# Kernel optimization log

Measured on AMD Instinct MI355X. Metric: run time of the kernel, lower is better.

The kernel has to match this reference:

```python
import jax, jax.numpy as jnp
import numpy as np

IN_CH = 1024
OUT_CH = 1024
N_SUBJECTS = 32
B = 512


def setup_inputs() -> dict:
    key = jax.random.key(0)
    k_x, k_w, k_b, k_idx = jax.random.split(key, 4)
    scale = 1.0 / (IN_CH ** 0.5)
    x = jax.random.normal(k_x, (B, IN_CH), dtype=jnp.float32)
    weights = jax.random.normal(k_w, (N_SUBJECTS, IN_CH, OUT_CH), dtype=jnp.float32) * scale
    bias = jax.random.normal(k_b, (N_SUBJECTS, OUT_CH), dtype=jnp.float32) * scale
    subject_idx = jax.random.randint(k_idx, (B,), 0, N_SUBJECTS, dtype=jnp.int64)
    return {"x": x, "subject_idx": subject_idx, "weights": weights, "bias": bias}


def reference(x, subject_idx, weights, bias):
    # gather per-sample weight [B,C,D] and bias [B,D]
    w = weights[subject_idx]          # [B, C, D]
    b = bias[subject_idx]             # [B, D]
    out = jnp.einsum('bc,bcd->bd', x, w) + b
    return out
```

## Files before the change

### kernel.cpp

```cpp
#include <hip/hip_runtime.h>
#include <hip/hip_bf16.h>


#define N_SUBJ 32
#define B_ROWS 512
#define IN_CH_K 1024
#define OUT_CH_K 1024
#define ROWS_PER_CHUNK 16
#define MAX_CHUNKS 64
#define CSEGS 4
#define CSEG 256
#define DTILES 4
#define DTILE 256

#define ENT_OFF 1
#define PERM_OFF 256
#define PART_OFF_F 1024
#define PART_FLOATS (CSEGS * B_ROWS * OUT_CH_K)
#define WS_NEED_BYTES (4096 + (size_t)PART_FLOATS * 4)

__global__ __launch_bounds__(512) void build_groups(
    const int* __restrict__ idx, int* __restrict__ ws)
{
    __shared__ int counts[N_SUBJ];
    __shared__ int offs[N_SUBJ];
    __shared__ int cursor[N_SUBJ];
    const int t = threadIdx.x;
    if (t < N_SUBJ) counts[t] = 0;
    __syncthreads();
    const int s = idx[t] & (N_SUBJ - 1);
    atomicAdd(&counts[s], 1);
    __syncthreads();
    if (t == 0) {
        int acc = 0, nch = 0;
        for (int i = 0; i < N_SUBJ; ++i) {
            offs[i] = acc;
            cursor[i] = acc;
            acc += counts[i];
        }
        for (int i = 0; i < N_SUBJ; ++i) {
            for (int st = 0; st < counts[i]; st += ROWS_PER_CHUNK) {
                int c = counts[i] - st;
                if (c > ROWS_PER_CHUNK) c = ROWS_PER_CHUNK;
                ws[ENT_OFF + nch * 3 + 0] = i;
                ws[ENT_OFF + nch * 3 + 1] = offs[i] + st;
                ws[ENT_OFF + nch * 3 + 2] = c;
                ++nch;
            }
        }
        ws[0] = nch;
    }
    __syncthreads();
    const int pos = atomicAdd(&cursor[s], 1);
    ws[PERM_OFF + pos] = t;
}

__global__ __launch_bounds__(256) void init_bias(
    const int* __restrict__ idx, const float* __restrict__ bias,
    float* __restrict__ out)
{
    const int b = blockIdx.x;
    const int s = idx[b];
    const int d = threadIdx.x * 4;
    *(float4*)&out[(size_t)b * OUT_CH_K + d] =
        *(const float4*)&bias[(size_t)s * OUT_CH_K + d];
}

template<bool ATOMIC>
__global__ __launch_bounds__(256) void subject_gemm(
    const float* __restrict__ x, const float* __restrict__ W,
    const int* __restrict__ ws, float* __restrict__ ws_part,
    float* __restrict__ out)
{
    const int chunk = blockIdx.x;
    if (chunk >= ws[0]) return;
    const int s     = ws[ENT_OFF + chunk * 3 + 0];
    const int start = ws[ENT_OFF + chunk * 3 + 1];
    const int cnt   = ws[ENT_OFF + chunk * 3 + 2];
    const int cbase = blockIdx.y * CSEG;
    const int dbase = blockIdx.z * DTILE;

    __shared__ float xs[ROWS_PER_CHUNK][CSEG];
    __shared__ int rowidx[ROWS_PER_CHUNK];

    const int t = threadIdx.x;
    if (t < ROWS_PER_CHUNK)
        rowidx[t] = (t < cnt) ? ws[PERM_OFF + start + t] : -1;
    __syncthreads();

    #pragma unroll
    for (int i = 0; i < ROWS_PER_CHUNK; ++i) {
        const int r = rowidx[i];
        xs[i][t] = (r >= 0) ? x[(size_t)r * IN_CH_K + cbase + t] : 0.0f;
    }
    __syncthreads();

    const int lane = t & 63;
    const int wave = t >> 6;
    const int d    = dbase + lane * 4;
    const int r0   = wave * 4;

    float4 acc0 = make_float4(0.f, 0.f, 0.f, 0.f);
    float4 acc1 = make_float4(0.f, 0.f, 0.f, 0.f);
    float4 acc2 = make_float4(0.f, 0.f, 0.f, 0.f);
    float4 acc3 = make_float4(0.f, 0.f, 0.f, 0.f);

    const float* wbase = W + ((size_t)s * IN_CH_K * OUT_CH_K)
                           + (size_t)cbase * OUT_CH_K + d;

    for (int cb = 0; cb < CSEG; cb += 8) {
        float4 wbuf[8];
        #pragma unroll
        for (int j = 0; j < 8; ++j)
            wbuf[j] = *(const float4*)(wbase + (size_t)(cb + j) * OUT_CH_K);
        #pragma unroll
        for (int j = 0; j < 8; ++j) {
            const float xv0 = xs[r0 + 0][cb + j];
            const float xv1 = xs[r0 + 1][cb + j];
            const float xv2 = xs[r0 + 2][cb + j];
            const float xv3 = xs[r0 + 3][cb + j];
            const float4 w4 = wbuf[j];
            acc0.x += xv0 * w4.x; acc0.y += xv0 * w4.y;
            acc0.z += xv0 * w4.z; acc0.w += xv0 * w4.w;
            acc1.x += xv1 * w4.x; acc1.y += xv1 * w4.y;
            acc1.z += xv1 * w4.z; acc1.w += xv1 * w4.w;
            acc2.x += xv2 * w4.x; acc2.y += xv2 * w4.y;
            acc2.z += xv2 * w4.z; acc2.w += xv2 * w4.w;
            acc3.x += xv3 * w4.x; acc3.y += xv3 * w4.y;
            acc3.z += xv3 * w4.z; acc3.w += xv3 * w4.w;
        }
    }

    float4 accs[4] = {acc0, acc1, acc2, acc3};
    #pragma unroll
    for (int r = 0; r < 4; ++r) {
        const int rr = r0 + r;
        if (rr < cnt) {
            const size_t row = (size_t)rowidx[rr];
            if (ATOMIC) {
                float* o = &out[row * OUT_CH_K + d];
                atomicAdd(o + 0, accs[r].x);
                atomicAdd(o + 1, accs[r].y);
                atomicAdd(o + 2, accs[r].z);
                atomicAdd(o + 3, accs[r].w);
            } else {
                *(float4*)&ws_part[((size_t)blockIdx.y * B_ROWS + row)
                                   * OUT_CH_K + d] = accs[r];
            }
        }
    }
}

__global__ __launch_bounds__(256) void reduce_parts(
    const int* __restrict__ idx, const float* __restrict__ bias,
    const float* __restrict__ part, float* __restrict__ out)
{
    const int b = blockIdx.x;
    const int s = idx[b];
    const int d = threadIdx.x * 4;
    float4 a = *(const float4*)&bias[(size_t)s * OUT_CH_K + d];
    #pragma unroll
    for (int k = 0; k < CSEGS; ++k) {
        const float4 p = *(const float4*)
            &part[((size_t)k * B_ROWS + b) * OUT_CH_K + d];
        a.x += p.x; a.y += p.y; a.z += p.z; a.w += p.w;
    }
    *(float4*)&out[(size_t)b * OUT_CH_K + d] = a;
}

extern "C" void kernel_launch(void* const* d_in, const int* in_sizes, int n_in,
                              void* d_out, int out_size, void* d_ws, size_t ws_size,
                              hipStream_t stream) {
    const float* x    = (const float*)d_in[0];
    const int*   idx  = (const int*)d_in[1];
    const float* W    = (const float*)d_in[2];
    const float* bias = (const float*)d_in[3];
    float* out = (float*)d_out;
    int* ws = (int*)d_ws;
    float* ws_part = (float*)ws + PART_OFF_F;

    build_groups<<<1, 512, 0, stream>>>(idx, ws);

    dim3 grid(MAX_CHUNKS, CSEGS, DTILES);
    if (ws_size >= WS_NEED_BYTES) {
        subject_gemm<false><<<grid, 256, 0, stream>>>(x, W, ws, ws_part, out);
        reduce_parts<<<B_ROWS, 256, 0, stream>>>(idx, bias, ws_part, out);
    } else {
        init_bias<<<B_ROWS, 256, 0, stream>>>(idx, bias, out);
        subject_gemm<true><<<grid, 256, 0, stream>>>(x, W, ws, ws_part, out);
    }
}
```

Measured before the change: 251.9 us.

## Double-buffer weight loads with inline asm and drop LDS staging of x

Rewrites the per-subject GEMM inner loop. Weight float4 loads are issued through inline global_load_dwordx4 with explicit vmcnt waits, alternating two register buffers so the next rows load while the current ones are multiplied. x values are now read directly from global memory per wave instead of being staged in shared memory, which removes the block barriers and lets waves with no rows exit early. The C dimension is split into 8 segments of 128 instead of 4 of 256, doubling the grid and the number of partial buffers the reduction has to read. The risks are a fragile hand-written wait schedule that ignores the compiler's own vmcnt tracking for the x loads, and extra partial-sum traffic; reduce_parts and the workspace size check now depend on CSEGS=8.

```diff
diff --git a/kernel.cpp b/kernel.cpp
--- a/kernel.cpp
+++ b/kernel.cpp
@@ -1,6 +1,8 @@
 #include <hip/hip_runtime.h>
 #include <hip/hip_bf16.h>
 
+
+typedef float f4v __attribute__((ext_vector_type(4)));
 
 #define N_SUBJ 32
 #define B_ROWS 512
@@ -8,8 +10,8 @@
 #define OUT_CH_K 1024
 #define ROWS_PER_CHUNK 16
 #define MAX_CHUNKS 64
-#define CSEGS 4
-#define CSEG 256
+#define CSEGS 8
+#define CSEG 128
 #define DTILES 4
 #define DTILE 256
 
@@ -66,6 +68,15 @@
         *(const float4*)&bias[(size_t)s * OUT_CH_K + d];
 }
 
+#define GLOAD(dst, ptr) \
+    asm volatile("global_load_dwordx4 %0, %1, off" \
+                 : "=v"(dst) : "v"(ptr) : "memory")
+#define WAIT_VM(n) do { \
+    asm volatile("s_waitcnt vmcnt(" #n ")" ::: "memory"); \
+    __builtin_amdgcn_sched_barrier(0); } while (0)
+#define FMA4(acc, w0, w1, w2, w3, xv) \
+    acc += w0 * xv.x; acc += w1 * xv.y; acc += w2 * xv.z; acc += w3 * xv.w;
+
 template<bool ATOMIC>
 __global__ __launch_bounds__(256) void subject_gemm(
     const float* __restrict__ x, const float* __restrict__ W,
@@ -73,81 +84,112 @@
     float* __restrict__ out)
 {
     const int chunk = blockIdx.x;
-    if (chunk >= ws[0]) return;
-    const int s     = ws[ENT_OFF + chunk * 3 + 0];
-    const int start = ws[ENT_OFF + chunk * 3 + 1];
-    const int cnt   = ws[ENT_OFF + chunk * 3 + 2];
+    const int nch = __builtin_amdgcn_readfirstlane(ws[0]);
+    if (chunk >= nch) return;
+    const int s     = __builtin_amdgcn_readfirstlane(ws[ENT_OFF + chunk * 3 + 0]);
+    const int start = __builtin_amdgcn_readfirstlane(ws[ENT_OFF + chunk * 3 + 1]);
+    const int cnt   = __builtin_amdgcn_readfirstlane(ws[ENT_OFF + chunk * 3 + 2]);
     const int cbase = blockIdx.y * CSEG;
     const int dbase = blockIdx.z * DTILE;
 
-    __shared__ float xs[ROWS_PER_CHUNK][CSEG];
-    __shared__ int rowidx[ROWS_PER_CHUNK];
-
-    const int t = threadIdx.x;
-    if (t < ROWS_PER_CHUNK)
-        rowidx[t] = (t < cnt) ? ws[PERM_OFF + start + t] : -1;
-    __syncthreads();
+    const int t     = threadIdx.x;
+    const int lane  = t & 63;
+    const int wave  = t >> 6;
+    const int rbase = wave * 4;
+    if (rbase >= cnt) return;
+    const int nr = cnt - rbase;
+
+    const int r0 = __builtin_amdgcn_readfirstlane(ws[PERM_OFF + start + rbase + 0]);
+    const int r1 = (nr > 1) ? __builtin_amdgcn_readfirstlane(ws[PERM_OFF + start + rbase + 1]) : r0;
+    const int r2 = (nr > 2) ? __builtin_amdgcn_readfirstlane(ws[PERM_OFF + start + rbase + 2]) : r0;
+    const int r3 = (nr > 3) ? __builtin_amdgcn_readfirstlane(ws[PERM_OFF + start + rbase + 3]) : r0;
+
+    const float* xr0 = x + (size_t)r0 * IN_CH_K + cbase;
+    const float* xr1 = x + (size_t)r1 * IN_CH_K + cbase;
+    const float* xr2 = x + (size_t)r2 * IN_CH_K + cbase;
+    const float* xr3 = x + (size_t)r3 * IN_CH_K + cbase;
+
+    const int d = dbase + lane * 4;
+    const float* wp = W + (size_t)s * IN_CH_K * OUT_CH_K
+                        + (size_t)cbase * OUT_CH_K + d;
+
+    f4v acc0 = {0.f, 0.f, 0.f, 0.f};
+    f4v acc1 = {0.f, 0.f, 0.f, 0.f};
+    f4v acc2 = {0.f, 0.f, 0.f, 0.f};
+    f4v acc3 = {0.f, 0.f, 0.f, 0.f};
+    f4v wa0, wa1, wa2, wa3, wb0, wb1, wb2, wb3;
+
+    WAIT_VM(0);
+
+    GLOAD(wa0, wp + 0 * OUT_CH_K);
+    GLOAD(wa1, wp + 1 * OUT_CH_K);
+    GLOAD(wa2, wp + 2 * OUT_CH_K);
+    GLOAD(wa3, wp + 3 * OUT_CH_K);
 
     #pragma unroll
-    for (int i = 0; i < ROWS_PER_CHUNK; ++i) {
-        const int r = rowidx[i];
-        xs[i][t] = (r >= 0) ? x[(size_t)r * IN_CH_K + cbase + t] : 0.0f;
-    }
-    __syncthreads();
-
-    const int lane = t & 63;
-    const int wave = t >> 6;
-    const int d    = dbase + lane * 4;
-    const int r0   = wave * 4;
-
-    float4 acc0 = make_float4(0.f, 0.f, 0.f, 0.f);
-    float4 acc1 = make_float4(0.f, 0.f, 0.f, 0.f);
-    float4 acc2 = make_float4(0.f, 0.f, 0.f, 0.f);
-    float4 acc3 = make_float4(0.f, 0.f, 0.f, 0.f);
-
-    const float* wbase = W + ((size_t)s * IN_CH_K * OUT_CH_K)
-                           + (size_t)cbase * OUT_CH_K + d;
-
     for (int cb = 0; cb < CSEG; cb += 8) {
-        float4 wbuf[8];
-        #pragma unroll
-        for (int j = 0; j < 8; ++j)
-            wbuf[j] = *(const float4*)(wbase + (size_t)(cb + j) * OUT_CH_K);
-        #pragma unroll
-        for (int j = 0; j < 8; ++j) {
-            const float xv0 = xs[r0 + 0][cb + j];
-            const float xv1 = xs[r0 + 1][cb + j];
-            const float xv2 = xs[r0 + 2][cb + j];
-            const float xv3 = xs[r0 + 3][cb + j];
-            const float4 w4 = wbuf[j];
-            acc0.x += xv0 * w4.x; acc0.y += xv0 * w4.y;
-            acc0.z += xv0 * w4.z; acc0.w += xv0 * w4.w;
-            acc1.x += xv1 * w4.x; acc1.y += xv1 * w4.y;
-            acc1.z += xv1 * w4.z; acc1.w += xv1 * w4.w;
-            acc2.x += xv2 * w4.x; acc2.y += xv2 * w4.y;
-            acc2.z += xv2 * w4.z; acc2.w += xv2 * w4.w;
-            acc3.x += xv3 * w4.x; acc3.y += xv3 * w4.y;
-            acc3.z += xv3 * w4.z; acc3.w += xv3 * w4.w;
-        }
-    }
-
-    float4 accs[4] = {acc0, acc1, acc2, acc3};
-    #pragma unroll
-    for (int r = 0; r < 4; ++r) {
-        const int rr = r0 + r;
-        if (rr < cnt) {
-            const size_t row = (size_t)rowidx[rr];
-            if (ATOMIC) {
-                float* o = &out[row * OUT_CH_K + d];
-                atomicAdd(o + 0, accs[r].x);
-                atomicAdd(o + 1, accs[r].y);
-                atomicAdd(o + 2, accs[r].z);
-                atomicAdd(o + 3, accs[r].w);
-            } else {
-                *(float4*)&ws_part[((size_t)blockIdx.y * B_ROWS + row)
-                                   * OUT_CH_K + d] = accs[r];
-            }
-        }
+        {
+            const float* wq = wp + (size_t)(cb + 4) * OUT_CH_K;
+            GLOAD(wb0, wq + 0 * OUT_CH_K);
+            GLOAD(wb1, wq + 1 * OUT_CH_K);
+            GLOAD(wb2, wq + 2 * OUT_CH_K);
+            GLOAD(wb3, wq + 3 * OUT_CH_K);
+        }
+        const float4 xa0 = *(const float4*)(xr0 + cb);
+        const float4 xa1 = *(const float4*)(xr1 + cb);
+        const float4 xa2 = *(const float4*)(xr2 + cb);
+        const float4 xa3 = *(const float4*)(xr3 + cb);
+        WAIT_VM(4);
+        FMA4(acc0, wa0, wa1, wa2, wa3, xa0)
+        FMA4(acc1, wa0, wa1, wa2, wa3, xa1)
+        FMA4(acc2, wa0, wa1, wa2, wa3, xa2)
+        FMA4(acc3, wa0, wa1, wa2, wa3, xa3)
+
+        const float4 xb0 = *(const float4*)(xr0 + cb + 4);
+        const float4 xb1 = *(const float4*)(xr1 + cb + 4);
+        const float4 xb2 = *(const float4*)(xr2 + cb + 4);
+        const float4 xb3 = *(const float4*)(xr3 + cb + 4);
+        if (cb + 8 < CSEG) {
+            const float* wr = wp + (size_t)(cb + 8) * OUT_CH_K;
+            GLOAD(wa0, wr + 0 * OUT_CH_K);
+            GLOAD(wa1, wr + 1 * OUT_CH_K);
+            GLOAD(wa2, wr + 2 * OUT_CH_K);
+            GLOAD(wa3, wr + 3 * OUT_CH_K);
+            WAIT_VM(4);
+        } else {
+            WAIT_VM(0);
+        }
+        FMA4(acc0, wb0, wb1, wb2, wb3, xb0)
+        FMA4(acc1, wb0, wb1, wb2, wb3, xb1)
+        FMA4(acc2, wb0, wb1, wb2, wb3, xb2)
+        FMA4(acc3, wb0, wb1, wb2, wb3, xb3)
+    }
+
+    if (ATOMIC) {
+        float* o0 = &out[(size_t)r0 * OUT_CH_K + d];
+        atomicAdd(o0 + 0, acc0.x); atomicAdd(o0 + 1, acc0.y);
+        atomicAdd(o0 + 2, acc0.z); atomicAdd(o0 + 3, acc0.w);
+        if (nr > 1) {
+            float* o = &out[(size_t)r1 * OUT_CH_K + d];
+            atomicAdd(o + 0, acc1.x); atomicAdd(o + 1, acc1.y);
+            atomicAdd(o + 2, acc1.z); atomicAdd(o + 3, acc1.w);
+        }
+        if (nr > 2) {
+            float* o = &out[(size_t)r2 * OUT_CH_K + d];
+            atomicAdd(o + 0, acc2.x); atomicAdd(o + 1, acc2.y);
+            atomicAdd(o + 2, acc2.z); atomicAdd(o + 3, acc2.w);
+        }
+        if (nr > 3) {
+            float* o = &out[(size_t)r3 * OUT_CH_K + d];
+            atomicAdd(o + 0, acc3.x); atomicAdd(o + 1, acc3.y);
+            atomicAdd(o + 2, acc3.z); atomicAdd(o + 3, acc3.w);
+        }
+    } else {
+        float* pb = ws_part + (size_t)blockIdx.y * B_ROWS * OUT_CH_K + d;
+        *(f4v*)(pb + (size_t)r0 * OUT_CH_K) = acc0;
+        if (nr > 1) *(f4v*)(pb + (size_t)r1 * OUT_CH_K) = acc1;
+        if (nr > 2) *(f4v*)(pb + (size_t)r2 * OUT_CH_K) = acc2;
+        if (nr > 3) *(f4v*)(pb + (size_t)r3 * OUT_CH_K) = acc3;
     }
 }
 
```

Result: slower. 642.8 us (+155.2%).

## Split C across waves so each W element is loaded once per block

Applied to the files above, without the earlier changes.

Reassigns work so each of the four waves handles a 64-channel slice of the C segment for all 16 rows, instead of each wave covering 4 rows over the whole segment. This removes the fourfold redundant loading of weight tiles per block. Weight loads are double-buffered with inline asm loads and explicit vmcnt waits to overlap memory with FMAs. The per-wave partial sums are then reduced through shared memory with several barriers, at the cost of higher register pressure (16 float4 accumulators).

```diff
diff --git a/kernel.cpp b/kernel.cpp
--- a/kernel.cpp
+++ b/kernel.cpp
@@ -1,6 +1,8 @@
 #include <hip/hip_runtime.h>
 #include <hip/hip_bf16.h>
 
+
+typedef float f4v __attribute__((ext_vector_type(4)));
 
 #define N_SUBJ 32
 #define B_ROWS 512
@@ -10,8 +12,10 @@
 #define MAX_CHUNKS 64
 #define CSEGS 4
 #define CSEG 256
+#define WSLICE 64
 #define DTILES 4
 #define DTILE 256
+#define XPAD 20
 
 #define ENT_OFF 1
 #define PERM_OFF 256
@@ -66,8 +70,28 @@
         *(const float4*)&bias[(size_t)s * OUT_CH_K + d];
 }
 
+#define GLOAD(dst, ptr) \
+    asm volatile("global_load_dwordx4 %0, %1, off" : "=v"(dst) : "v"(ptr))
+#define WAIT_VM(n) do { \
+    asm volatile("s_waitcnt vmcnt(" #n ")" ::: "memory"); \
+    __builtin_amdgcn_sched_barrier(0); } while (0)
+
+#define CSTEP(wreg, cidx) { \
+    const float4 x0 = ((const float4*)&xst[cidx][0])[0]; \
+    const float4 x1 = ((const float4*)&xst[cidx][0])[1]; \
+    const float4 x2 = ((const float4*)&xst[cidx][0])[2]; \
+    const float4 x3 = ((const float4*)&xst[cidx][0])[3]; \
+    acc[ 0] += wreg * x0.x;  acc[ 1] += wreg * x0.y; \
+    acc[ 2] += wreg * x0.z;  acc[ 3] += wreg * x0.w; \
+    acc[ 4] += wreg * x1.x;  acc[ 5] += wreg * x1.y; \
+    acc[ 6] += wreg * x1.z;  acc[ 7] += wreg * x1.w; \
+    acc[ 8] += wreg * x2.x;  acc[ 9] += wreg * x2.y; \
+    acc[10] += wreg * x2.z;  acc[11] += wreg * x2.w; \
+    acc[12] += wreg * x3.x;  acc[13] += wreg * x3.y; \
+    acc[14] += wreg * x3.z;  acc[15] += wreg * x3.w; }
+
 template<bool ATOMIC>
-__global__ __launch_bounds__(256) void subject_gemm(
+__global__ __launch_bounds__(256, 3) void subject_gemm(
     const float* __restrict__ x, const float* __restrict__ W,
     const int* __restrict__ ws, float* __restrict__ ws_part,
     float* __restrict__ out)
@@ -80,7 +104,7 @@
     const int cbase = blockIdx.y * CSEG;
     const int dbase = blockIdx.z * DTILE;
 
-    __shared__ float xs[ROWS_PER_CHUNK][CSEG];
+    __shared__ float xst[CSEG][XPAD];
     __shared__ int rowidx[ROWS_PER_CHUNK];
 
     const int t = threadIdx.x;
@@ -89,63 +113,102 @@
     __syncthreads();
 
     #pragma unroll
-    for (int i = 0; i < ROWS_PER_CHUNK; ++i) {
-        const int r = rowidx[i];
-        xs[i][t] = (r >= 0) ? x[(size_t)r * IN_CH_K + cbase + t] : 0.0f;
+    for (int r = 0; r < ROWS_PER_CHUNK; ++r) {
+        const int row = rowidx[r];
+        xst[t][r] = (row >= 0) ? x[(size_t)row * IN_CH_K + cbase + t] : 0.0f;
     }
     __syncthreads();
 
     const int lane = t & 63;
     const int wave = t >> 6;
+    const int cs   = wave * WSLICE;
     const int d    = dbase + lane * 4;
-    const int r0   = wave * 4;
-
-    float4 acc0 = make_float4(0.f, 0.f, 0.f, 0.f);
-    float4 acc1 = make_float4(0.f, 0.f, 0.f, 0.f);
-    float4 acc2 = make_float4(0.f, 0.f, 0.f, 0.f);
-    float4 acc3 = make_float4(0.f, 0.f, 0.f, 0.f);
-
-    const float* wbase = W + ((size_t)s * IN_CH_K * OUT_CH_K)
-                           + (size_t)cbase * OUT_CH_K + d;
-
-    for (int cb = 0; cb < CSEG; cb += 8) {
-        float4 wbuf[8];
+    const float* wp = W + (size_t)s * (IN_CH_K * OUT_CH_K)
+                        + (size_t)(cbase + cs) * OUT_CH_K + d;
+
+    f4v acc[16];
+    #pragma unroll
+    for (int r = 0; r < 16; ++r) acc[r] = (f4v){0.f, 0.f, 0.f, 0.f};
+    f4v wa0, wa1, wa2, wa3, wb0, wb1, wb2, wb3;
+
+    GLOAD(wa0, wp + 0 * OUT_CH_K);
+    GLOAD(wa1, wp + 1 * OUT_CH_K);
+    GLOAD(wa2, wp + 2 * OUT_CH_K);
+    GLOAD(wa3, wp + 3 * OUT_CH_K);
+    GLOAD(wb0, wp + 4 * OUT_CH_K);
+    GLOAD(wb1, wp + 5 * OUT_CH_K);
+    GLOAD(wb2, wp + 6 * OUT_CH_K);
+    GLOAD(wb3, wp + 7 * OUT_CH_K);
+
+    #pragma unroll 1
+    for (int cb = 0; cb < WSLICE - 8; cb += 8) {
+        WAIT_VM(4);
+        CSTEP(wa0, cs + cb + 0)
+        CSTEP(wa1, cs + cb + 1)
+        CSTEP(wa2, cs + cb + 2)
+        CSTEP(wa3, cs + cb + 3)
+        const float* wn = wp + (size_t)(cb + 8) * OUT_CH_K;
+        GLOAD(wa0, wn + 0 * OUT_CH_K);
+        GLOAD(wa1, wn + 1 * OUT_CH_K);
+        GLOAD(wa2, wn + 2 * OUT_CH_K);
+        GLOAD(wa3, wn + 3 * OUT_CH_K);
+        WAIT_VM(4);
+        CSTEP(wb0, cs + cb + 4)
+        CSTEP(wb1, cs + cb + 5)
+        CSTEP(wb2, cs + cb + 6)
+        CSTEP(wb3, cs + cb + 7)
+        GLOAD(wb0, wn + 4 * OUT_CH_K);
+        GLOAD(wb1, wn + 5 * OUT_CH_K);
+        GLOAD(wb2, wn + 6 * OUT_CH_K);
+        GLOAD(wb3, wn + 7 * OUT_CH_K);
+    }
+    {
+        const int cb = WSLICE - 8;
+        WAIT_VM(4);
+        CSTEP(wa0, cs + cb + 0)
+        CSTEP(wa1, cs + cb + 1)
+        CSTEP(wa2, cs + cb + 2)
+        CSTEP(wa3, cs + cb + 3)
+        WAIT_VM(0);
+        CSTEP(wb0, cs + cb + 4)
+        CSTEP(wb1, cs + cb + 5)
+        CSTEP(wb2, cs + cb + 6)
+        CSTEP(wb3, cs + cb + 7)
+    }
+
+    __syncthreads();
+    float (*obuf)[DTILE] = (float(*)[DTILE])&xst[0][0];
+    if (wave == 0) {
         #pragma unroll
-        for (int j = 0; j < 8; ++j)
-            wbuf[j] = *(const float4*)(wbase + (size_t)(cb + j) * OUT_CH_K);
-        #pragma unroll
-        for (int j = 0; j < 8; ++j) {
-            const float xv0 = xs[r0 + 0][cb + j];
-            const float xv1 = xs[r0 + 1][cb + j];
-            const float xv2 = xs[r0 + 2][cb + j];
-            const float xv3 = xs[r0 + 3][cb + j];
-            const float4 w4 = wbuf[j];
-            acc0.x += xv0 * w4.x; acc0.y += xv0 * w4.y;
-            acc0.z += xv0 * w4.z; acc0.w += xv0 * w4.w;
-            acc1.x += xv1 * w4.x; acc1.y += xv1 * w4.y;
-            acc1.z += xv1 * w4.z; acc1.w += xv1 * w4.w;
-            acc2.x += xv2 * w4.x; acc2.y += xv2 * w4.y;
-            acc2.z += xv2 * w4.z; acc2.w += xv2 * w4.w;
-            acc3.x += xv3 * w4.x; acc3.y += xv3 * w4.y;
-            acc3.z += xv3 * w4.z; acc3.w += xv3 * w4.w;
-        }
-    }
-
-    float4 accs[4] = {acc0, acc1, acc2, acc3};
-    #pragma unroll
-    for (int r = 0; r < 4; ++r) {
-        const int rr = r0 + r;
-        if (rr < cnt) {
-            const size_t row = (size_t)rowidx[rr];
+        for (int r = 0; r < 16; ++r)
+            *(f4v*)&obuf[r][lane * 4] = acc[r];
+    }
+    __syncthreads();
+    #pragma unroll
+    for (int w = 1; w < 4; ++w) {
+        if (wave == w) {
+            #pragma unroll
+            for (int r = 0; r < 16; ++r) {
+                f4v v = *(const f4v*)&obuf[r][lane * 4];
+                *(f4v*)&obuf[r][lane * 4] = v + acc[r];
+            }
+        }
+        __syncthreads();
+    }
+
+    #pragma unroll
+    for (int i = 0; i < 4; ++i) {
+        const int r = wave * 4 + i;
+        const int row = rowidx[r];
+        if (row >= 0) {
+            const f4v v = *(const f4v*)&obuf[r][lane * 4];
             if (ATOMIC) {
-                float* o = &out[row * OUT_CH_K + d];
-                atomicAdd(o + 0, accs[r].x);
-                atomicAdd(o + 1, accs[r].y);
-                atomicAdd(o + 2, accs[r].z);
-                atomicAdd(o + 3, accs[r].w);
+                float* o = &out[(size_t)row * OUT_CH_K + d];
+                atomicAdd(o + 0, v.x); atomicAdd(o + 1, v.y);
+                atomicAdd(o + 2, v.z); atomicAdd(o + 3, v.w);
             } else {
-                *(float4*)&ws_part[((size_t)blockIdx.y * B_ROWS + row)
-                                   * OUT_CH_K + d] = accs[r];
+                *(f4v*)&ws_part[((size_t)blockIdx.y * B_ROWS + row)
+                                * OUT_CH_K + d] = v;
             }
         }
     }
```

After: 226.3 us. -10.2%, faster.
